# Kernel tuning notes

Hardware: AMD Instinct MI355X
Metric: run time of the kernel (lower is better)

## Reference

```python
import jax, jax.numpy as jnp
import numpy as np

B, S, T = 2, 1024, 1024          # batch, new tokens, cache length (prefill: S == T)
DIM, NH, NKV, HD = 2048, 16, 4, 128
FFN = 5632
EPS = 1e-5
STD = 0.02


def rms_norm(x, w, eps=EPS):
    return x * jax.lax.rsqrt(jnp.mean(x * x, axis=-1, keepdims=True) + eps) * w


def apply_rope(x, freqs_cis):
    # x: [B, S, H, HD]; freqs_cis: [S, HD//2, 2] (cos, sin) over consecutive pairs
    xr = x.reshape(*x.shape[:-1], HD // 2, 2)
    cos = freqs_cis[None, :, None, :, 0]
    sin = freqs_cis[None, :, None, :, 1]
    x0, x1 = xr[..., 0], xr[..., 1]
    rot = jnp.stack([x0 * cos - x1 * sin, x0 * sin + x1 * cos], axis=-1)
    return rot.reshape(x.shape)


def setup_inputs() -> dict:
    key = jax.random.key(0)
    ks = jax.random.split(key, 10)
    x = jax.random.normal(ks[0], (B, S, DIM), jnp.float32)
    # rotary tables
    inv_freq = 1.0 / (10000.0 ** (np.arange(0, HD, 2, dtype=np.float32) / HD))
    ang = np.outer(np.arange(S, dtype=np.float32), inv_freq)          # [S, HD//2]
    freqs_cis = jnp.asarray(np.stack([np.cos(ang), np.sin(ang)], -1), jnp.float32)
    cache_k = jnp.zeros((1, B, T, NKV, HD), jnp.float32)
    cache_v = jnp.zeros((1, B, T, NKV, HD), jnp.float32)
    mask = jnp.triu(jnp.full((S, T), -1e9, jnp.float32), k=1)         # additive causal
    wq = jax.random.normal(ks[1], (DIM, NH, HD), jnp.float32) * STD
    wk = jax.random.normal(ks[2], (DIM, NKV, HD), jnp.float32) * STD
    wv = jax.random.normal(ks[3], (DIM, NKV, HD), jnp.float32) * STD
    wo = jax.random.normal(ks[4], (NH * HD, DIM), jnp.float32) * STD
    w_gate = jax.random.normal(ks[5], (DIM, FFN), jnp.float32) * STD
    w_up = jax.random.normal(ks[6], (DIM, FFN), jnp.float32) * STD
    w_down = jax.random.normal(ks[7], (FFN, DIM), jnp.float32) * STD
    attn_norm_w = jnp.ones((DIM,), jnp.float32)
    ffn_norm_w = jnp.ones((DIM,), jnp.float32)
    return dict(x=x, freqs_cis=freqs_cis, cache_k=cache_k, cache_v=cache_v,
                mask=mask, wq=wq, wk=wk, wv=wv, wo=wo, w_gate=w_gate,
                w_up=w_up, w_down=w_down, attn_norm_w=attn_norm_w,
                ffn_norm_w=ffn_norm_w, layer_idx=0)


def reference(x, freqs_cis, cache_k, cache_v, mask, wq, wk, wv, wo,
              w_gate, w_up, w_down, attn_norm_w, ffn_norm_w, layer_idx):
    # --- attention sub-block ---
    h = rms_norm(x, attn_norm_w)
    q = jnp.einsum('bsd,dhk->bshk', h, wq)          # [B,S,NH,HD]
    k = jnp.einsum('bsd,dgk->bsgk', h, wk)          # [B,S,NKV,HD]
    v = jnp.einsum('bsd,dgk->bsgk', h, wv)
    q = apply_rope(q, freqs_cis)
    k = apply_rope(k, freqs_cis)
    # append to per-layer KV cache at position 0 (prefill)
    cache_k = jax.lax.dynamic_update_slice(cache_k, k[None], (layer_idx, 0, 0, 0, 0))
    cache_v = jax.lax.dynamic_update_slice(cache_v, v[None], (layer_idx, 0, 0, 0, 0))
    keys = cache_k[layer_idx]                        # [B,T,NKV,HD]
    vals = cache_v[layer_idx]
    J = NH // NKV                                    # query heads per kv head
    qg = q.reshape(B, S, NKV, J, HD)
    scale = 1.0 / jnp.sqrt(jnp.float32(HD))
    scores = jnp.einsum('bsgjd,btgd->bgjst', qg, keys) * scale  # [B,NKV,J,S,T]
    scores = scores + mask                           # broadcast [S,T]
    probs = jax.nn.softmax(scores, axis=-1)
    ctx = jnp.einsum('bgjst,btgd->bsgjd', probs, vals).reshape(B, S, NH * HD)
    x = x + ctx @ wo
    # --- SwiGLU FFN sub-block ---
    hf = rms_norm(x, ffn_norm_w)
    ffn = (jax.nn.silu(hf @ w_gate) * (hf @ w_up)) @ w_down
    x = x + ffn
    return (x, cache_k, cache_v)
```

## Files before the change

### kernel.cpp

```cpp
#include <hip/hip_runtime.h>

typedef float f32x4 __attribute__((ext_vector_type(4)));
typedef __bf16 bf16x8 __attribute__((ext_vector_type(8)));
typedef unsigned short u16;

#define DIM 2048
#define SEQ 1024
#define BSZ 2
#define NH 16
#define NKV 4
#define HD 128
#define FFNDIM 5632
#define MROWS (BSZ * SEQ)

__device__ __forceinline__ u16 f2bf(float f) {
  union { float f; unsigned u; } v; v.f = f;
  unsigned u = v.u;
  unsigned r = (u + 0x7fffu + ((u >> 16) & 1u)) >> 16;
  return (u16)r;
}
__device__ __forceinline__ float bf2f(u16 h) {
  union { unsigned u; float f; } v; v.u = ((unsigned)h) << 16; return v.f;
}

__device__ __forceinline__ void gld16(const void* g, void* l) {
  __builtin_amdgcn_global_load_lds(
      (const __attribute__((address_space(1))) unsigned int*)g,
      (__attribute__((address_space(3))) unsigned int*)l, 16, 0, 0);
}

__global__ __launch_bounds__(256) void kxpose(const float* __restrict__ W,
                                              u16* __restrict__ Wt,
                                              int K, int N, int rs, int ro) {
  __shared__ float t[64][65];
  int kb = blockIdx.y * 64, nb = blockIdx.x * 64;
  int tid = threadIdx.x;
#pragma unroll
  for (int it = 0; it < 16; ++it) {
    int idx = it * 256 + tid;
    int r = idx >> 6, c = idx & 63;
    t[r][c] = W[(size_t)(kb + r) * N + nb + c];
  }
  __syncthreads();
#pragma unroll
  for (int it = 0; it < 16; ++it) {
    int idx = it * 256 + tid;
    int rn = idx >> 6, ck = idx & 63;
    Wt[((size_t)(nb + rn) * rs + ro) * K + kb + ck] = f2bf(t[ck][rn]);
  }
}

__global__ __launch_bounds__(256) void kvxpose(const u16* __restrict__ v,
                                               u16* __restrict__ vt) {
  __shared__ u16 t[64][66];
  int bg = blockIdx.z;
  int b = bg >> 2, g = bg & 3;
  int s0 = blockIdx.x * 64, d0 = blockIdx.y * 64;
  int tid = threadIdx.x;
  int rr = tid >> 4, cc = (tid & 15) * 4;
#pragma unroll
  for (int it = 0; it < 4; ++it) {
    int r = it * 16 + rr;
    *(uint2*)&t[r][cc] =
        *(const uint2*)(v + (size_t)(b * SEQ + s0 + r) * (NKV * HD) + g * HD + d0 + cc);
  }
  __syncthreads();
#pragma unroll
  for (int it = 0; it < 4; ++it) {
    int r = it * 16 + rr;
    u16 o[4] = {t[cc][r], t[cc + 1][r], t[cc + 2][r], t[cc + 3][r]};
    *(uint2*)(vt + (size_t)((b * NKV + g) * HD + d0 + r) * SEQ + s0 + cc) = *(const uint2*)o;
  }
}

__global__ __launch_bounds__(256) void krmsnorm(const float* __restrict__ x,
                                                const float* __restrict__ w,
                                                u16* __restrict__ out) {
  int row = blockIdx.x, tid = threadIdx.x;
  const float* xr = x + (size_t)row * DIM;
  float4 a = *(const float4*)(xr + tid * 8);
  float4 b = *(const float4*)(xr + tid * 8 + 4);
  float ss = a.x * a.x + a.y * a.y + a.z * a.z + a.w * a.w +
             b.x * b.x + b.y * b.y + b.z * b.z + b.w * b.w;
#pragma unroll
  for (int off = 1; off < 64; off <<= 1) ss += __shfl_xor(ss, off, 64);
  __shared__ float red[4];
  if ((tid & 63) == 0) red[tid >> 6] = ss;
  __syncthreads();
  float tot = red[0] + red[1] + red[2] + red[3];
  float sc = rsqrtf(tot * (1.0f / DIM) + 1e-5f);
  float xs[8] = {a.x, a.y, a.z, a.w, b.x, b.y, b.z, b.w};
  const float* wr = w + tid * 8;
  u16 o[8];
#pragma unroll
  for (int j = 0; j < 8; ++j) o[j] = f2bf(xs[j] * sc * wr[j]);
  *(int4*)(out + (size_t)row * DIM + tid * 8) = *(const int4*)o;
}

template <int EPI>
__global__ __launch_bounds__(512, 4) void kgemm(
    const u16* __restrict__ A, const u16* __restrict__ Bt, int N, int K,
    u16* o0, u16* __restrict__ o1, u16* __restrict__ o2,
    float* of, const float* res, const float* __restrict__ fc) {
  __shared__ u16 As[2][128 * 64];
  __shared__ u16 Bs[2][128 * 64];
  int bn = blockIdx.x * 128, bm = blockIdx.y * 128;
  int tid = threadIdx.x, lane = tid & 63, wv = tid >> 6;
  int wm = (wv >> 2) * 64;
  int wn = (wv & 3) * 32;
  int r16 = lane & 15, grp = lane >> 4;
  int srow = lane >> 3;
  int schunk = ((lane & 7) ^ srow) * 8;
  f32x4 acc[4][2] = {};
  const u16* Abase = A + (size_t)(bm + wv * 16) * K + schunk;
  const u16* Bbase = Bt + (size_t)(bn + wv * 16) * K + schunk;
  int woff = wv * 16 * 64;

  auto STAGE = [&](int buf, int k0) {
#pragma unroll
    for (int j = 0; j < 2; ++j) {
      gld16(Abase + (size_t)(j * 8 + srow) * K + k0, &As[buf][woff + j * 512]);
      gld16(Bbase + (size_t)(j * 8 + srow) * K + k0, &Bs[buf][woff + j * 512]);
    }
  };
  auto COMPUTE = [&](int buf) {
#pragma unroll
    for (int kk = 0; kk < 2; ++kk) {
      int swz = (((kk << 2) | grp) ^ (r16 & 7)) * 8;
      bf16x8 af[4], bfr[2];
#pragma unroll
      for (int m = 0; m < 4; ++m)
        af[m] = *(const bf16x8*)&As[buf][(wm + m * 16 + r16) * 64 + swz];
#pragma unroll
      for (int n = 0; n < 2; ++n)
        bfr[n] = *(const bf16x8*)&Bs[buf][(wn + n * 16 + r16) * 64 + swz];
#pragma unroll
      for (int m = 0; m < 4; ++m)
#pragma unroll
        for (int n = 0; n < 2; ++n)
          acc[m][n] = __builtin_amdgcn_mfma_f32_16x16x32_bf16(af[m], bfr[n], acc[m][n], 0, 0, 0);
    }
  };

  STAGE(0, 0);
  int nt = K >> 6;
  for (int t = 0; t < nt; ++t) {
    int cur = t & 1;
    if (t + 1 < nt) {
      STAGE(cur ^ 1, (t + 1) << 6);
      asm volatile("s_waitcnt vmcnt(4)" ::: "memory");
    } else {
      asm volatile("s_waitcnt vmcnt(0)" ::: "memory");
    }
    __builtin_amdgcn_sched_barrier(0);
    __builtin_amdgcn_s_barrier();
    __builtin_amdgcn_sched_barrier(0);
    COMPUTE(cur);
    __builtin_amdgcn_s_barrier();
  }

  bool oddlane = (r16 & 1) != 0;
#pragma unroll
  for (int mi = 0; mi < 4; ++mi) {
#pragma unroll
    for (int ni = 0; ni < 2; ++ni) {
#pragma unroll
      for (int r = 0; r < 4; ++r) {
        int gr = bm + wm + mi * 16 + grp * 4 + r;
        int gc = bn + wn + ni * 16 + r16;
        float v = acc[mi][ni][r];
        if constexpr (EPI == 0) {
          float pv = __shfl_xor(v, 1, 64);
          if (gc < DIM + 512) {
            int s_idx = gr & (SEQ - 1);
            int jp = (gc & 127) >> 1;
            float2 cs = *(const float2*)(fc + s_idx * HD + jp * 2);
            float y;
            if (oddlane) y = pv * cs.y + v * cs.x;
            else         y = v * cs.x - pv * cs.y;
            if (gc < DIM) {
              o0[(size_t)gr * DIM + gc] = f2bf(y);
            } else {
              int c2 = gc - DIM;
              o1[(size_t)gr * 512 + c2] = f2bf(y);
              ((float*)res)[(size_t)gr * 512 + c2] = y;
            }
          } else {
            int c2 = gc - (DIM + 512);
            of[(size_t)gr * 512 + c2] = v;
            o2[(size_t)gr * 512 + c2] = f2bf(v);
          }
        } else {
          of[(size_t)gr * N + gc] = v + res[(size_t)gr * N + gc];
        }
      }
    }
  }
}

__global__ __launch_bounds__(512, 4) void kgemm_gu(
    const u16* __restrict__ A, const u16* __restrict__ Bt,
    u16* __restrict__ out) {
  const int K = DIM;
  __shared__ u16 As[2][128 * 64];
  __shared__ u16 Bs[2][128 * 64];
  int bn = blockIdx.x * 128, bm = blockIdx.y * 128;
  int tid = threadIdx.x, lane = tid & 63, wv = tid >> 6;
  int wm = (wv >> 2) * 64;
  int wn = (wv & 3) * 32;
  int r16 = lane & 15, grp = lane >> 4;
  int srow = lane >> 3;
  int schunk = ((lane & 7) ^ srow) * 8;
  f32x4 acc[4][2] = {};
  const u16* Abase = A + (size_t)(bm + wv * 16) * K + schunk;
  const u16* Bbase = Bt + (size_t)(bn + wv * 16) * K + schunk;
  int woff = wv * 16 * 64;

  auto STAGE = [&](int buf, int k0) {
#pragma unroll
    for (int j = 0; j < 2; ++j) {
      gld16(Abase + (size_t)(j * 8 + srow) * K + k0, &As[buf][woff + j * 512]);
      gld16(Bbase + (size_t)(j * 8 + srow) * K + k0, &Bs[buf][woff + j * 512]);
    }
  };
  auto COMPUTE = [&](int buf) {
#pragma unroll
    for (int kk = 0; kk < 2; ++kk) {
      int swz = (((kk << 2) | grp) ^ (r16 & 7)) * 8;
      bf16x8 af[4], bfr[2];
#pragma unroll
      for (int m = 0; m < 4; ++m)
        af[m] = *(const bf16x8*)&As[buf][(wm + m * 16 + r16) * 64 + swz];
#pragma unroll
      for (int n = 0; n < 2; ++n)
        bfr[n] = *(const bf16x8*)&Bs[buf][(wn + n * 16 + r16) * 64 + swz];
#pragma unroll
      for (int m = 0; m < 4; ++m)
#pragma unroll
        for (int n = 0; n < 2; ++n)
          acc[m][n] = __builtin_amdgcn_mfma_f32_16x16x32_bf16(af[m], bfr[n], acc[m][n], 0, 0, 0);
    }
  };

  STAGE(0, 0);
  int nt = K >> 6;
  for (int t = 0; t < nt; ++t) {
    int cur = t & 1;
    if (t + 1 < nt) {
      STAGE(cur ^ 1, (t + 1) << 6);
      asm volatile("s_waitcnt vmcnt(4)" ::: "memory");
    } else {
      asm volatile("s_waitcnt vmcnt(0)" ::: "memory");
    }
    __builtin_amdgcn_sched_barrier(0);
    __builtin_amdgcn_s_barrier();
    __builtin_amdgcn_sched_barrier(0);
    COMPUTE(cur);
    __builtin_amdgcn_s_barrier();
  }

  bool evenlane = (r16 & 1) == 0;
#pragma unroll
  for (int mi = 0; mi < 4; ++mi) {
#pragma unroll
    for (int ni = 0; ni < 2; ++ni) {
#pragma unroll
      for (int r = 0; r < 4; ++r) {
        float v = acc[mi][ni][r];
        float pv = __shfl_xor(v, 1, 64);
        if (evenlane) {
          int gr = bm + wm + mi * 16 + grp * 4 + r;
          int gc = bn + wn + ni * 16 + r16;
          float sg = v / (1.0f + __expf(-v));
          out[(size_t)gr * FFNDIM + (gc >> 1)] = f2bf(sg * pv);
        }
      }
    }
  }
}

__global__ __launch_bounds__(256) void kattn(const u16* __restrict__ qb,
                                             const u16* __restrict__ kb,
                                             const u16* __restrict__ vtb,
                                             u16* __restrict__ ctxb) {
  __shared__ u16 Ks[2][64 * 128];
  __shared__ u16 Vs[2][128 * 64];
  __shared__ u16 Plds[4][16][72];
  int tid = threadIdx.x;
  int l = tid & 63, wv = tid >> 6;
  int qg = 15 - blockIdx.x;
  int h = blockIdx.y, b = blockIdx.z;
  int g = h >> 2;
  int q0 = qg * 64 + wv * 16;
  int r16 = l & 15, grp = l >> 4;
  const float scale = 0.08838834764831845f;
  bf16x8 qf[4];
  {
    const u16* qrow = qb + (size_t)(b * SEQ + q0 + r16) * DIM + h * HD + grp * 8;
#pragma unroll
    for (int c = 0; c < 4; ++c) qf[c] = *(const bf16x8*)(qrow + c * 32);
  }
  const u16* kg = kb + (size_t)b * SEQ * (NKV * HD) + g * HD;
  const u16* vg = vtb + (size_t)((b * NKV + g) * HD) * SEQ;

  auto STAGE = [&](int buf, int t0) {
#pragma unroll
    for (int p = 0; p < 4; ++p) {
      int row = p * 16 + wv * 4 + (l >> 4);
      int ch = (l & 15) ^ (row & 7);
      gld16(kg + (size_t)(t0 + row) * (NKV * HD) + ch * 8,
            &Ks[buf][p * 2048 + wv * 512]);
    }
#pragma unroll
    for (int p = 0; p < 4; ++p) {
      int row = p * 32 + wv * 8 + (l >> 3);
      int ch = (l & 7) ^ (row & 7);
      gld16(vg + (size_t)row * SEQ + t0 + ch * 8,
            &Vs[buf][p * 2048 + wv * 512]);
    }
  };

  f32x4 ctx[8] = {};
  float m = -1e30f, lsum = 0.0f;
  int q_idx = q0 + r16;
  int ntiles = qg + 1;

  STAGE(0, 0);
  for (int tt = 0; tt < ntiles; ++tt) {
    int cur = tt & 1;
    if (tt + 1 < ntiles) {
      STAGE(cur ^ 1, (tt + 1) * 64);
      asm volatile("s_waitcnt vmcnt(8)" ::: "memory");
    } else {
      asm volatile("s_waitcnt vmcnt(0)" ::: "memory");
    }
    __builtin_amdgcn_sched_barrier(0);
    __builtin_amdgcn_s_barrier();
    __builtin_amdgcn_sched_barrier(0);
    int t0 = tt * 64;
    f32x4 d[4] = {{0.f, 0.f, 0.f, 0.f}, {0.f, 0.f, 0.f, 0.f},
                  {0.f, 0.f, 0.f, 0.f}, {0.f, 0.f, 0.f, 0.f}};
    __builtin_amdgcn_s_setprio(1);
#pragma unroll
    for (int c = 0; c < 4; ++c) {
#pragma unroll
      for (int ch = 0; ch < 4; ++ch) {
        int row = ch * 16 + r16;
        bf16x8 kf = *(const bf16x8*)&Ks[cur][row * 128 + (((c * 4 + grp) ^ (row & 7)) * 8)];
        d[ch] = __builtin_amdgcn_mfma_f32_16x16x32_bf16(kf, qf[c], d[ch], 0, 0, 0);
      }
    }
    __builtin_amdgcn_s_setprio(0);
    float p[16];
    float mx = -1e30f;
#pragma unroll
    for (int ch = 0; ch < 4; ++ch) {
#pragma unroll
      for (int r = 0; r < 4; ++r) {
        int tA = t0 + ch * 16 + grp * 4 + r;
        float s = d[ch][r] * scale;
        if (tA > q_idx) s = -1e30f;
        p[ch * 4 + r] = s;
        mx = fmaxf(mx, s);
      }
    }
    mx = fmaxf(mx, __shfl_xor(mx, 16, 64));
    mx = fmaxf(mx, __shfl_xor(mx, 32, 64));
    if (!__all(mx - m <= 8.0f)) {
      float mnew = fmaxf(m, mx);
      float corr = __expf(m - mnew);
      lsum *= corr;
      float cf[4];
#pragma unroll
      for (int r = 0; r < 4; ++r) cf[r] = __shfl(corr, grp * 4 + r, 64);
#pragma unroll
      for (int dc = 0; dc < 8; ++dc)
#pragma unroll
        for (int r = 0; r < 4; ++r) ctx[dc][r] *= cf[r];
      m = mnew;
    }
    float psum = 0.f;
#pragma unroll
    for (int i = 0; i < 16; ++i) {
      p[i] = __expf(p[i] - m);
      psum += p[i];
    }
    psum += __shfl_xor(psum, 16, 64);
    psum += __shfl_xor(psum, 32, 64);
    lsum += psum;
#pragma unroll
    for (int ch = 0; ch < 4; ++ch) {
      unsigned w0 = (unsigned)f2bf(p[ch * 4]) | ((unsigned)f2bf(p[ch * 4 + 1]) << 16);
      unsigned w1 = (unsigned)f2bf(p[ch * 4 + 2]) | ((unsigned)f2bf(p[ch * 4 + 3]) << 16);
      *(unsigned*)&Plds[wv][r16][ch * 16 + grp * 4] = w0;
      *(unsigned*)&Plds[wv][r16][ch * 16 + grp * 4 + 2] = w1;
    }
    bf16x8 pa0, pa1;
    {
      union { bf16x8 v; int4 q; } u0, u1;
      u0.q = *(const int4*)&Plds[wv][r16][grp * 8];
      u1.q = *(const int4*)&Plds[wv][r16][32 + grp * 8];
      pa0 = u0.v;
      pa1 = u1.v;
    }
    __builtin_amdgcn_s_setprio(1);
#pragma unroll
    for (int dc = 0; dc < 8; ++dc) {
      int row = dc * 16 + r16;
      bf16x8 vf0 = *(const bf16x8*)&Vs[cur][row * 64 + ((grp ^ (row & 7)) * 8)];
      bf16x8 vf1 = *(const bf16x8*)&Vs[cur][row * 64 + (((grp + 4) ^ (row & 7)) * 8)];
      ctx[dc] = __builtin_amdgcn_mfma_f32_16x16x32_bf16(pa0, vf0, ctx[dc], 0, 0, 0);
      ctx[dc] = __builtin_amdgcn_mfma_f32_16x16x32_bf16(pa1, vf1, ctx[dc], 0, 0, 0);
    }
    __builtin_amdgcn_s_setprio(0);
    __builtin_amdgcn_s_barrier();
  }
  float linv = 1.0f / lsum;
  float lf[4];
#pragma unroll
  for (int r = 0; r < 4; ++r) lf[r] = __shfl(linv, grp * 4 + r, 64);
  u16* crow = ctxb + (size_t)(b * SEQ + q0) * DIM + h * HD;
#pragma unroll
  for (int dc = 0; dc < 8; ++dc)
#pragma unroll
    for (int r = 0; r < 4; ++r)
      crow[(size_t)(grp * 4 + r) * DIM + dc * 16 + r16] = f2bf(ctx[dc][r] * lf[r]);
}

extern "C" void kernel_launch(void* const* d_in, const int* in_sizes, int n_in,
                              void* d_out, int out_size, void* d_ws, size_t ws_size,
                              hipStream_t stream) {
  const float* x = (const float*)d_in[0];
  const float* fc = (const float*)d_in[1];
  const float* wq = (const float*)d_in[5];
  const float* wk = (const float*)d_in[6];
  const float* wv = (const float*)d_in[7];
  const float* wo = (const float*)d_in[8];
  const float* wg = (const float*)d_in[9];
  const float* wu = (const float*)d_in[10];
  const float* wd = (const float*)d_in[11];
  const float* anw = (const float*)d_in[12];
  const float* fnw = (const float*)d_in[13];

  float* out_x = (float*)d_out;
  float* out_ck = out_x + (size_t)MROWS * DIM;
  float* out_cv = out_ck + (size_t)MROWS * NKV * HD;

  char* ws = (char*)d_ws;
  u16* h_b    = (u16*)(ws);
  u16* q_b    = (u16*)(ws + (8u << 20));
  u16* k_b    = (u16*)(ws + (16u << 20));
  u16* v_b    = (u16*)(ws + (18u << 20));
  u16* ctx_b  = (u16*)(ws + (20u << 20));
  u16* hf_b   = (u16*)(ws + (28u << 20));
  u16* Wt     = (u16*)(ws + (60u << 20));
  u16* vt_b   = h_b;
  u16* Wt_gu  = (u16*)(ws + (36u << 20));
  u16* g_b    = (u16*)(ws);
  u16* Wt_dn  = (u16*)(ws + (36u << 20));

  kxpose<<<dim3(2048 / 64, 2048 / 64), 256, 0, stream>>>(wq, Wt, 2048, 2048, 1, 0);
  kxpose<<<dim3(512 / 64, 2048 / 64), 256, 0, stream>>>(wk, Wt + (size_t)2048 * 2048, 2048, 512, 1, 0);
  kxpose<<<dim3(512 / 64, 2048 / 64), 256, 0, stream>>>(wv, Wt + (size_t)2560 * 2048, 2048, 512, 1, 0);

  krmsnorm<<<MROWS, 256, 0, stream>>>(x, anw, h_b);
  kgemm<0><<<dim3(3072 / 128, 16), 512, 0, stream>>>(h_b, Wt, 3072, 2048,
                                                     q_b, k_b, v_b, out_cv, out_ck, fc);
  kvxpose<<<dim3(SEQ / 64, HD / 64, BSZ * NKV), 256, 0, stream>>>(v_b, vt_b);
  kattn<<<dim3(SEQ / 64, NH, BSZ), 256, 0, stream>>>(q_b, k_b, vt_b, ctx_b);

  kxpose<<<dim3(32, 32), 256, 0, stream>>>(wo, Wt, 2048, 2048, 1, 0);
  kgemm<2><<<dim3(16, 16), 512, 0, stream>>>(ctx_b, Wt, 2048, 2048,
                                             nullptr, nullptr, nullptr, out_x, x, nullptr);
  krmsnorm<<<MROWS, 256, 0, stream>>>(out_x, fnw, hf_b);

  kxpose<<<dim3(5632 / 64, 2048 / 64), 256, 0, stream>>>(wg, Wt_gu, 2048, 5632, 2, 0);
  kxpose<<<dim3(5632 / 64, 2048 / 64), 256, 0, stream>>>(wu, Wt_gu, 2048, 5632, 2, 1);
  kgemm_gu<<<dim3(11264 / 128, 16), 512, 0, stream>>>(hf_b, Wt_gu, g_b);
  kxpose<<<dim3(2048 / 64, 5632 / 64), 256, 0, stream>>>(wd, Wt_dn, 5632, 2048, 1, 0);
  kgemm<2><<<dim3(16, 16), 512, 0, stream>>>(g_b, Wt_dn, 2048, 5632,
                                             nullptr, nullptr, nullptr, out_x, out_x, nullptr);
}
```

Baseline: 377.8 us.

## Fuse V transpose into QKV GEMM epilogue and vectorize weight transpose

```diff
diff --git a/kernel.cpp b/kernel.cpp
--- a/kernel.cpp
+++ b/kernel.cpp
@@ -36,40 +36,21 @@
   int kb = blockIdx.y * 64, nb = blockIdx.x * 64;
   int tid = threadIdx.x;
 #pragma unroll
-  for (int it = 0; it < 16; ++it) {
+  for (int it = 0; it < 4; ++it) {
     int idx = it * 256 + tid;
-    int r = idx >> 6, c = idx & 63;
-    t[r][c] = W[(size_t)(kb + r) * N + nb + c];
+    int r = idx >> 4, c4 = (idx & 15) * 4;
+    float4 v = *(const float4*)(W + (size_t)(kb + r) * N + nb + c4);
+    t[r][c4] = v.x; t[r][c4 + 1] = v.y; t[r][c4 + 2] = v.z; t[r][c4 + 3] = v.w;
   }
   __syncthreads();
 #pragma unroll
-  for (int it = 0; it < 16; ++it) {
+  for (int it = 0; it < 4; ++it) {
     int idx = it * 256 + tid;
-    int rn = idx >> 6, ck = idx & 63;
-    Wt[((size_t)(nb + rn) * rs + ro) * K + kb + ck] = f2bf(t[ck][rn]);
-  }
-}
-
-__global__ __launch_bounds__(256) void kvxpose(const u16* __restrict__ v,
-                                               u16* __restrict__ vt) {
-  __shared__ u16 t[64][66];
-  int bg = blockIdx.z;
-  int b = bg >> 2, g = bg & 3;
-  int s0 = blockIdx.x * 64, d0 = blockIdx.y * 64;
-  int tid = threadIdx.x;
-  int rr = tid >> 4, cc = (tid & 15) * 4;
-#pragma unroll
-  for (int it = 0; it < 4; ++it) {
-    int r = it * 16 + rr;
-    *(uint2*)&t[r][cc] =
-        *(const uint2*)(v + (size_t)(b * SEQ + s0 + r) * (NKV * HD) + g * HD + d0 + cc);
-  }
-  __syncthreads();
-#pragma unroll
-  for (int it = 0; it < 4; ++it) {
-    int r = it * 16 + rr;
-    u16 o[4] = {t[cc][r], t[cc + 1][r], t[cc + 2][r], t[cc + 3][r]};
-    *(uint2*)(vt + (size_t)((b * NKV + g) * HD + d0 + r) * SEQ + s0 + cc) = *(const uint2*)o;
+    int rn = idx >> 4, ck4 = (idx & 15) * 4;
+    u16 o[4];
+#pragma unroll
+    for (int j = 0; j < 4; ++j) o[j] = f2bf(t[ck4 + j][rn]);
+    *(uint2*)(Wt + ((size_t)(nb + rn) * rs + ro) * K + kb + ck4) = *(const uint2*)o;
   }
 }
 
@@ -164,20 +145,21 @@
   for (int mi = 0; mi < 4; ++mi) {
 #pragma unroll
     for (int ni = 0; ni < 2; ++ni) {
-#pragma unroll
-      for (int r = 0; r < 4; ++r) {
-        int gr = bm + wm + mi * 16 + grp * 4 + r;
+      if constexpr (EPI == 0) {
         int gc = bn + wn + ni * 16 + r16;
-        float v = acc[mi][ni][r];
-        if constexpr (EPI == 0) {
-          float pv = __shfl_xor(v, 1, 64);
-          if (gc < DIM + 512) {
-            int s_idx = gr & (SEQ - 1);
-            int jp = (gc & 127) >> 1;
-            float2 cs = *(const float2*)(fc + s_idx * HD + jp * 2);
+        int gr0 = bm + wm + mi * 16 + grp * 4;
+        if (gc < DIM + 512) {
+          int s0 = gr0 & (SEQ - 1);
+          int jp = (gc & 127) >> 1;
+#pragma unroll
+          for (int r = 0; r < 4; ++r) {
+            float v = acc[mi][ni][r];
+            float pv = __shfl_xor(v, 1, 64);
+            float2 cs = *(const float2*)(fc + (s0 + r) * HD + jp * 2);
             float y;
             if (oddlane) y = pv * cs.y + v * cs.x;
             else         y = v * cs.x - pv * cs.y;
+            int gr = gr0 + r;
             if (gc < DIM) {
               o0[(size_t)gr * DIM + gc] = f2bf(y);
             } else {
@@ -185,13 +167,26 @@
               o1[(size_t)gr * 512 + c2] = f2bf(y);
               ((float*)res)[(size_t)gr * 512 + c2] = y;
             }
-          } else {
-            int c2 = gc - (DIM + 512);
-            of[(size_t)gr * 512 + c2] = v;
-            o2[(size_t)gr * 512 + c2] = f2bf(v);
           }
         } else {
-          of[(size_t)gr * N + gc] = v + res[(size_t)gr * N + gc];
+          int c2 = gc - (DIM + 512);
+          int g = c2 >> 7, d = c2 & 127;
+          int b = gr0 >> 10, s0 = gr0 & (SEQ - 1);
+          u16 o4[4];
+#pragma unroll
+          for (int r = 0; r < 4; ++r) {
+            float v = acc[mi][ni][r];
+            of[(size_t)(gr0 + r) * 512 + c2] = v;
+            o4[r] = f2bf(v);
+          }
+          *(uint2*)(o2 + ((size_t)(b * NKV + g) * HD + d) * SEQ + s0) = *(const uint2*)o4;
+        }
+      } else {
+#pragma unroll
+        for (int r = 0; r < 4; ++r) {
+          int gr = bm + wm + mi * 16 + grp * 4 + r;
+          int gc = bn + wn + ni * 16 + r16;
+          of[(size_t)gr * N + gc] = acc[mi][ni][r] + res[(size_t)gr * N + gc];
         }
       }
     }
@@ -450,11 +445,10 @@
   u16* h_b    = (u16*)(ws);
   u16* q_b    = (u16*)(ws + (8u << 20));
   u16* k_b    = (u16*)(ws + (16u << 20));
-  u16* v_b    = (u16*)(ws + (18u << 20));
   u16* ctx_b  = (u16*)(ws + (20u << 20));
+  u16* vt_b   = (u16*)(ws + (28u << 20));
   u16* hf_b   = (u16*)(ws + (28u << 20));
   u16* Wt     = (u16*)(ws + (60u << 20));
-  u16* vt_b   = h_b;
   u16* Wt_gu  = (u16*)(ws + (36u << 20));
   u16* g_b    = (u16*)(ws);
   u16* Wt_dn  = (u16*)(ws + (36u << 20));
@@ -465,8 +459,7 @@
 
   krmsnorm<<<MROWS, 256, 0, stream>>>(x, anw, h_b);
   kgemm<0><<<dim3(3072 / 128, 16), 512, 0, stream>>>(h_b, Wt, 3072, 2048,
-                                                     q_b, k_b, v_b, out_cv, out_ck, fc);
-  kvxpose<<<dim3(SEQ / 64, HD / 64, BSZ * NKV), 256, 0, stream>>>(v_b, vt_b);
+                                                     q_b, k_b, vt_b, out_cv, out_ck, fc);
   kattn<<<dim3(SEQ / 64, NH, BSZ), 256, 0, stream>>>(q_b, k_b, vt_b, ctx_b);
 
   kxpose<<<dim3(32, 32), 256, 0, stream>>>(wo, Wt, 2048, 2048, 1, 0);
```

Result: no change. 372.4 us, median of 3 (-1.4%).
